# Performance work log

Hardware: AMD Instinct MI355X
Metric: run time of the kernel (lower is better)

## Reference

```python
import jax, jax.numpy as jnp
import numpy as np

N, K, F = 65536, 32, 128


def setup_inputs() -> dict:
    key = jax.random.key(0)
    k1, k2, k3, k4 = jax.random.split(key, 4)
    x = jax.random.normal(k1, (N, F), dtype=jnp.float32)
    means = jax.random.normal(k2, (K, F), dtype=jnp.float32)
    # lower-triangular Cholesky factors of precisions with strictly positive diagonal
    a = jax.random.normal(k3, (K, F, F), dtype=jnp.float32) * 0.05
    precisions_chol = jnp.tril(a, k=-1) + jnp.eye(F, dtype=jnp.float32)[None] * (
        1.0 + 0.1 * jax.random.uniform(k3, (K, 1, 1), dtype=jnp.float32)
    )
    # valid mixture weights on the simplex (log is taken in forward)
    u = jax.random.uniform(k4, (K,), dtype=jnp.float32) + 0.1
    weights = u / jnp.sum(u)
    return {"x": x, "means": means, "precisions_chol": precisions_chol, "weights": weights}


def reference(x, means, precisions_chol, weights):
    n_features = x.shape[1]
    # log|prec_chol_k| = sum of log diagonal entries  -> [K]
    log_det = jnp.sum(jnp.log(jnp.diagonal(precisions_chol, axis1=1, axis2=2)), axis=1)
    # whitened residuals: (x - mu_k) @ P_k  done as two batched GEMMs -> [N,K,F]
    y = jnp.einsum("nf,kfg->nkg", x, precisions_chol) - jnp.einsum(
        "kf,kfg->kg", means, precisions_chol
    )[None, :, :]
    log_prob = jnp.sum(y * y, axis=-1)  # Mahalanobis^2, [N,K]
    log2pi = jnp.log(jnp.asarray(2.0 * np.pi, dtype=x.dtype))
    log_gauss = -0.5 * (n_features * log2pi + log_prob) + log_det[None, :]
    # NLL-ish score: logsumexp over components with log mixture weights -> [N]
    return jax.nn.logsumexp(log_gauss + jnp.log(weights)[None, :], axis=1)
```

## Files before the change

kernel.cpp:

```cpp
#include <hip/hip_runtime.h>
#include <hip/hip_bf16.h>


#define NPTS 65536
#define KC 32
#define FD 128
#define SLABB 20480

typedef __attribute__((ext_vector_type(8))) short short8;
typedef __attribute__((ext_vector_type(8))) unsigned short ushort8;
typedef __attribute__((ext_vector_type(16))) float f32x16;

#define MFMA(A, B, C) __builtin_amdgcn_mfma_f32_32x32x16_bf16((A), (B), (C), 0, 0, 0)

static __device__ __forceinline__ unsigned short f2bf(float f) {
  unsigned int u = __float_as_uint(f);
  u += 0x7FFFu + ((u >> 16) & 1u);
  return (unsigned short)(u >> 16);
}

static __device__ __forceinline__ void gll(const unsigned char* g, unsigned char* l) {
  __builtin_amdgcn_global_load_lds((const __attribute__((address_space(1))) void*)g,
                                   (__attribute__((address_space(3))) void*)l, 16, 0, 0);
}

__global__ void prep12(const float* __restrict__ means, const float* __restrict__ P,
                       const float* __restrict__ w, float* __restrict__ v,
                       float* __restrict__ ck3) {
  int k = blockIdx.x, g = threadIdx.x;
  const float* Pk = P + k * FD * FD;
  float acc = 0.f;
  for (int f = 0; f < FD; ++f) acc = fmaf(means[k * FD + f], Pk[f * FD + g], acc);
  __shared__ float smp[FD], r1[FD], r2[FD];
  smp[g] = acc;
  r1[g] = logf(Pk[g * FD + g]);
  r2[g] = acc * acc;
  __syncthreads();
  const float* Pr = Pk + g * FD;
  float a2 = 0.f;
  for (int j = 0; j < FD; ++j) a2 = fmaf(Pr[j], smp[j], a2);
  v[k * FD + g] = a2;
  for (int off = 64; off; off >>= 1) {
    if (g < off) { r1[g] += r1[g + off]; r2[g] += r2[g + off]; }
    __syncthreads();
  }
  if (g == 0)
    ck3[k] = logf(w[k]) + r1[0] - 0.5f * ((float)FD * 1.8378770664093453f + r2[0]);
}

__global__ void prep3(const float* __restrict__ v, unsigned char* __restrict__ Ximg) {
  int id = blockIdx.x * 256 + threadIdx.x;
  int l = id & 63, s = id >> 6;
  int r = l & 31, f0 = 16 * s + 8 * (l >> 5);
  ushort8 o;
#pragma unroll
  for (int j = 0; j < 8; ++j) o[j] = f2bf(v[r * FD + f0 + j]);
  *(ushort8*)(Ximg + (size_t)id * 16) = o;
}

__global__ void prep4(const float* __restrict__ P, unsigned char* __restrict__ Aimg) {
  int id = blockIdx.x * 256 + threadIdx.x;
  int l = id & 63;
  int c = (id >> 6) % 20;
  int k = id / 1280;
  int q, s;
  if (c < 8)       { q = 0; s = c; }
  else if (c < 10) { q = 3; s = c - 2; }
  else if (c < 16) { q = 1; s = c - 8; }
  else             { q = 2; s = c - 12; }
  int g = q * 32 + (l & 31);
  int f0 = 16 * s + 8 * (l >> 5);
  ushort8 o;
#pragma unroll
  for (int j = 0; j < 8; ++j) o[j] = f2bf(P[k * 16384 + (f0 + j) * 128 + g]);
  *(ushort8*)(Aimg + (size_t)id * 16) = o;
}

__global__ __launch_bounds__(256, 2) void gmm_main(const float* __restrict__ x,
                                                   const unsigned char* __restrict__ Aimg,
                                                   const unsigned char* __restrict__ Ximg,
                                                   const float* __restrict__ ck3,
                                                   float* __restrict__ out) {
  __shared__ __align__(16) unsigned char abuf[2 * SLABB];
  __shared__ __align__(16) float xch[2][4][32];
  __shared__ float ck[KC];
  const int tid = threadIdx.x;
  const int wid = tid >> 6;
  const int lane = tid & 63;
  const int half = lane >> 5;
  const int ln = lane & 31;
  const int p = wid & 1;
  const int nq = wid >> 1;
  const int nbase = blockIdx.x * 128;

  if (tid < KC) ck[tid] = ck3[tid];

  {
    const unsigned char* gx = Ximg + wid * 2048 + lane * 16;
    unsigned char* lx = abuf + SLABB + wid * 2048;
    gll(gx, lx);
    gll(gx + 1024, lx + 1024);
    const unsigned char* gs = Aimg + wid * 5120 + lane * 16;
    unsigned char* ls = abuf + wid * 5120;
#pragma unroll
    for (int i = 0; i < 5; ++i) gll(gs + i * 1024, ls + i * 1024);
  }

  short8 xf[2][8];
#pragma unroll
  for (int t = 0; t < 2; ++t) {
    const float* xr = x + (size_t)(nbase + nq * 64 + t * 32 + ln) * FD + 8 * half;
#pragma unroll
    for (int s = 0; s < 8; ++s) {
      const float4 a = *(const float4*)(xr + 16 * s);
      const float4 b = *(const float4*)(xr + 16 * s + 4);
      short8 f;
      f[0] = (short)f2bf(a.x); f[1] = (short)f2bf(a.y);
      f[2] = (short)f2bf(a.z); f[3] = (short)f2bf(a.w);
      f[4] = (short)f2bf(b.x); f[5] = (short)f2bf(b.y);
      f[6] = (short)f2bf(b.z); f[7] = (short)f2bf(b.w);
      xf[t][s] = f;
    }
  }

  f32x16 zc;
#pragma unroll
  for (int i = 0; i < 16; ++i) zc[i] = 0.f;

  asm volatile("s_waitcnt vmcnt(0)" ::: "memory");
  __syncthreads();

  f32x16 xv;
  {
    const unsigned char* xb = abuf + SLABB + lane * 16;
    {
      const short8 fx = *(const short8*)xb;
      xv = MFMA(fx, p ? xf[1][0] : xf[0][0], zc);
    }
#pragma unroll
    for (int s = 1; s < 8; ++s) {
      const short8 fx = *(const short8*)(xb + s * 1024);
      xv = MFMA(fx, p ? xf[1][s] : xf[0][s], xv);
    }
  }
  __syncthreads();

  float m = -__builtin_inff(), ssum = 0.f;

  for (int k = 0; k < KC; ++k) {
    const int RB = (k & 1) * SLABB;
    const int WB = SLABB - RB;
    const int ph = k & 1;
    const unsigned char* rb = abuf + RB + p * 10240 + lane * 16;
    short8 fr[10];
#pragma unroll
    for (int i = 0; i < 10; ++i) fr[i] = *(const short8*)(rb + i * 1024);
    if (k + 1 < KC) {
      const unsigned char* gs = Aimg + (size_t)(k + 1) * SLABB + wid * 5120 + lane * 16;
      unsigned char* ls = abuf + WB + wid * 5120;
#pragma unroll
      for (int i = 0; i < 5; ++i) gll(gs + i * 1024, ls + i * 1024);
    }
    f32x16 a00, a01, a10, a11;
    __builtin_amdgcn_s_setprio(1);
    if (p == 0) {
      a00 = MFMA(fr[0], xf[0][0], zc);
      a01 = MFMA(fr[0], xf[1][0], zc);
#pragma unroll
      for (int s = 1; s < 8; ++s) {
        a00 = MFMA(fr[s], xf[0][s], a00);
        a01 = MFMA(fr[s], xf[1][s], a01);
      }
      a10 = MFMA(fr[8], xf[0][6], zc);
      a11 = MFMA(fr[8], xf[1][6], zc);
      a10 = MFMA(fr[9], xf[0][7], a10);
      a11 = MFMA(fr[9], xf[1][7], a11);
    } else {
      a00 = MFMA(fr[0], xf[0][2], zc);
      a01 = MFMA(fr[0], xf[1][2], zc);
#pragma unroll
      for (int s = 1; s < 6; ++s) {
        a00 = MFMA(fr[s], xf[0][s + 2], a00);
        a01 = MFMA(fr[s], xf[1][s + 2], a01);
      }
      a10 = MFMA(fr[6], xf[0][4], zc);
      a11 = MFMA(fr[6], xf[1][4], zc);
#pragma unroll
      for (int j = 1; j < 4; ++j) {
        a10 = MFMA(fr[6 + j], xf[0][4 + j], a10);
        a11 = MFMA(fr[6 + j], xf[1][4 + j], a11);
      }
    }
    __builtin_amdgcn_s_setprio(0);
    float q0a = 0.f, q0b = 0.f, q1a = 0.f, q1b = 0.f;
#pragma unroll
    for (int i = 0; i < 16; ++i) {
      q0a = fmaf(a00[i], a00[i], q0a);
      q0b = fmaf(a10[i], a10[i], q0b);
      q1a = fmaf(a01[i], a01[i], q1a);
      q1b = fmaf(a11[i], a11[i], q1b);
    }
    float q0 = q0a + q0b, q1 = q1a + q1b;
    q0 += __shfl_xor(q0, 32, 64);
    q1 += __shfl_xor(q1, 32, 64);
    float sown = p ? q1 : q0;
    float soth = p ? q0 : q1;
    if (half == 0) xch[ph][wid ^ 1][ln] = soth;
    if (k + 1 < KC) asm volatile("s_waitcnt vmcnt(0)" ::: "memory");
    __syncthreads();
    float sfull = sown + xch[ph][wid][ln];
    const int owner = (k >> 2) & 1;
    const int idx = (k & 3) | ((k >> 3) << 2);
    float tx = (half == owner) ? xv[idx] : 0.f;
    tx += __shfl_xor(tx, 32, 64);
    sfull = fmaf(-2.f, tx, sfull);
    float vv = ck[k] - 0.5f * sfull;
    float nm = fmaxf(m, vv);
    ssum = ssum * __expf(m - nm) + __expf(vv - nm);
    m = nm;
  }

  if (half == 0) out[nbase + nq * 64 + p * 32 + ln] = m + logf(ssum);
}

extern "C" void kernel_launch(void* const* d_in, const int* in_sizes, int n_in,
                              void* d_out, int out_size, void* d_ws, size_t ws_size,
                              hipStream_t stream) {
  const float* x = (const float*)d_in[0];
  const float* means = (const float*)d_in[1];
  const float* P = (const float*)d_in[2];
  const float* w = (const float*)d_in[3];
  float* out = (float*)d_out;

  unsigned char* ws = (unsigned char*)d_ws;
  unsigned char* Aimg = ws;
  unsigned char* Ximg = ws + 655360;
  float* v = (float*)(ws + 655360 + 8192);
  float* ck3 = (float*)(ws + 655360 + 24576);

  prep12<<<32, 128, 0, stream>>>(means, P, w, v, ck3);
  prep3<<<2, 256, 0, stream>>>(v, Ximg);
  prep4<<<160, 256, 0, stream>>>(P, Aimg);
  gmm_main<<<NPTS / 128, 256, 0, stream>>>(x, Aimg, Ximg, ck3, out);
}
```

Baseline: 63.39 us.

## Fuse three prep kernels into one and use packed FMA for squared norms

Merges the mean-projection, Ximg packing and Aimg repacking prep kernels into a single per-component kernel that writes the bf16 images directly, removing two launches and the intermediate v buffer. The main kernel's sum of squares over MFMA accumulators now uses v_pk_fma_f32 through inline asm, handling two elements per instruction. The fused prep kernel uses only 32 blocks, so the Aimg repack runs with less parallelism than the former 160-block kernel. The Ximg writes are now scattered 2-byte stores.

```diff
diff --git a/kernel.cpp b/kernel.cpp
--- a/kernel.cpp
+++ b/kernel.cpp
@@ -10,6 +10,7 @@
 typedef __attribute__((ext_vector_type(8))) short short8;
 typedef __attribute__((ext_vector_type(8))) unsigned short ushort8;
 typedef __attribute__((ext_vector_type(16))) float f32x16;
+typedef __attribute__((ext_vector_type(2))) float f32x2;
 
 #define MFMA(A, B, C) __builtin_amdgcn_mfma_f32_32x32x16_bf16((A), (B), (C), 0, 0, 0)
 
@@ -24,56 +25,55 @@
                                    (__attribute__((address_space(3))) void*)l, 16, 0, 0);
 }
 
-__global__ void prep12(const float* __restrict__ means, const float* __restrict__ P,
-                       const float* __restrict__ w, float* __restrict__ v,
-                       float* __restrict__ ck3) {
-  int k = blockIdx.x, g = threadIdx.x;
+static __device__ __forceinline__ void pksq(f32x2& acc, float lo, float hi) {
+  f32x2 y;
+  y[0] = lo;
+  y[1] = hi;
+  asm("v_pk_fma_f32 %0, %1, %1, %0" : "+v"(acc) : "v"(y));
+}
+
+__global__ void prep_all(const float* __restrict__ means, const float* __restrict__ P,
+                         const float* __restrict__ w, unsigned char* __restrict__ Aimg,
+                         unsigned char* __restrict__ Ximg, float* __restrict__ ck3) {
+  const int k = blockIdx.x;
+  const int t = threadIdx.x;
   const float* Pk = P + k * FD * FD;
-  float acc = 0.f;
-  for (int f = 0; f < FD; ++f) acc = fmaf(means[k * FD + f], Pk[f * FD + g], acc);
   __shared__ float smp[FD], r1[FD], r2[FD];
-  smp[g] = acc;
-  r1[g] = logf(Pk[g * FD + g]);
-  r2[g] = acc * acc;
+  if (t < FD) {
+    float acc = 0.f;
+    for (int f = 0; f < FD; ++f) acc = fmaf(means[k * FD + f], Pk[f * FD + t], acc);
+    smp[t] = acc;
+    r1[t] = logf(Pk[t * FD + t]);
+    r2[t] = acc * acc;
+  }
   __syncthreads();
-  const float* Pr = Pk + g * FD;
-  float a2 = 0.f;
-  for (int j = 0; j < FD; ++j) a2 = fmaf(Pr[j], smp[j], a2);
-  v[k * FD + g] = a2;
+  if (t < FD) {
+    const float* Pr = Pk + t * FD;
+    float a2 = 0.f;
+    for (int j = 0; j < FD; ++j) a2 = fmaf(Pr[j], smp[j], a2);
+    const int id = ((t >> 4) * 64) + k + 32 * ((t >> 3) & 1);
+    *(unsigned short*)(Ximg + (size_t)id * 16 + (t & 7) * 2) = f2bf(a2);
+  }
   for (int off = 64; off; off >>= 1) {
-    if (g < off) { r1[g] += r1[g + off]; r2[g] += r2[g + off]; }
+    if (t < off) { r1[t] += r1[t + off]; r2[t] += r2[t + off]; }
     __syncthreads();
   }
-  if (g == 0)
+  if (t == 0)
     ck3[k] = logf(w[k]) + r1[0] - 0.5f * ((float)FD * 1.8378770664093453f + r2[0]);
-}
-
-__global__ void prep3(const float* __restrict__ v, unsigned char* __restrict__ Ximg) {
-  int id = blockIdx.x * 256 + threadIdx.x;
-  int l = id & 63, s = id >> 6;
-  int r = l & 31, f0 = 16 * s + 8 * (l >> 5);
-  ushort8 o;
-#pragma unroll
-  for (int j = 0; j < 8; ++j) o[j] = f2bf(v[r * FD + f0 + j]);
-  *(ushort8*)(Ximg + (size_t)id * 16) = o;
-}
-
-__global__ void prep4(const float* __restrict__ P, unsigned char* __restrict__ Aimg) {
-  int id = blockIdx.x * 256 + threadIdx.x;
-  int l = id & 63;
-  int c = (id >> 6) % 20;
-  int k = id / 1280;
-  int q, s;
-  if (c < 8)       { q = 0; s = c; }
-  else if (c < 10) { q = 3; s = c - 2; }
-  else if (c < 16) { q = 1; s = c - 8; }
-  else             { q = 2; s = c - 12; }
-  int g = q * 32 + (l & 31);
-  int f0 = 16 * s + 8 * (l >> 5);
-  ushort8 o;
-#pragma unroll
-  for (int j = 0; j < 8; ++j) o[j] = f2bf(P[k * 16384 + (f0 + j) * 128 + g]);
-  *(ushort8*)(Aimg + (size_t)id * 16) = o;
+  for (int i = t; i < 1280; i += 256) {
+    const int c = i >> 6, l = i & 63;
+    int q, s;
+    if (c < 8)       { q = 0; s = c; }
+    else if (c < 10) { q = 3; s = c - 2; }
+    else if (c < 16) { q = 1; s = c - 8; }
+    else             { q = 2; s = c - 12; }
+    const int g = q * 32 + (l & 31);
+    const int f0 = 16 * s + 8 * (l >> 5);
+    ushort8 o;
+#pragma unroll
+    for (int j = 0; j < 8; ++j) o[j] = f2bf(Pk[(f0 + j) * FD + g]);
+    *(ushort8*)(Aimg + (size_t)k * SLABB + (size_t)i * 16) = o;
+  }
 }
 
 __global__ __launch_bounds__(256, 2) void gmm_main(const float* __restrict__ x,
@@ -192,15 +192,18 @@
       }
     }
     __builtin_amdgcn_s_setprio(0);
-    float q0a = 0.f, q0b = 0.f, q1a = 0.f, q1b = 0.f;
-#pragma unroll
-    for (int i = 0; i < 16; ++i) {
-      q0a = fmaf(a00[i], a00[i], q0a);
-      q0b = fmaf(a10[i], a10[i], q0b);
-      q1a = fmaf(a01[i], a01[i], q1a);
-      q1b = fmaf(a11[i], a11[i], q1b);
-    }
-    float q0 = q0a + q0b, q1 = q1a + q1b;
+    f32x2 s0a, s0b, s1a, s1b;
+    s0a[0] = 0.f; s0a[1] = 0.f; s0b[0] = 0.f; s0b[1] = 0.f;
+    s1a[0] = 0.f; s1a[1] = 0.f; s1b[0] = 0.f; s1b[1] = 0.f;
+#pragma unroll
+    for (int i = 0; i < 8; ++i) {
+      pksq(s0a, a00[2 * i], a00[2 * i + 1]);
+      pksq(s0b, a10[2 * i], a10[2 * i + 1]);
+      pksq(s1a, a01[2 * i], a01[2 * i + 1]);
+      pksq(s1b, a11[2 * i], a11[2 * i + 1]);
+    }
+    float q0 = (s0a[0] + s0a[1]) + (s0b[0] + s0b[1]);
+    float q1 = (s1a[0] + s1a[1]) + (s1b[0] + s1b[1]);
     q0 += __shfl_xor(q0, 32, 64);
     q1 += __shfl_xor(q1, 32, 64);
     float sown = p ? q1 : q0;
@@ -235,11 +238,8 @@
   unsigned char* ws = (unsigned char*)d_ws;
   unsigned char* Aimg = ws;
   unsigned char* Ximg = ws + 655360;
-  float* v = (float*)(ws + 655360 + 8192);
-  float* ck3 = (float*)(ws + 655360 + 24576);
-
-  prep12<<<32, 128, 0, stream>>>(means, P, w, v, ck3);
-  prep3<<<2, 256, 0, stream>>>(v, Ximg);
-  prep4<<<160, 256, 0, stream>>>(P, Aimg);
+  float* ck3 = (float*)(ws + 655360 + 8192);
+
+  prep_all<<<32, 256, 0, stream>>>(means, P, w, Aimg, Ximg, ck3);
   gmm_main<<<NPTS / 128, 256, 0, stream>>>(x, Aimg, Ximg, ck3, out);
 }
```

Measured after the change: 65.76 us. +3.7%, slower.
